# Optimization experiments

Hardware: AMD Instinct MI355X
Metric: run time of the kernel (lower is better)

The kernel has to match this reference:

```python
import jax, jax.numpy as jnp
import numpy as np

N = 50000
E = 800000
D_IN = 128
D_H = 128


def setup_inputs() -> dict:
    key = jax.random.key(0)
    ks = jax.random.split(key, 12)
    x = jax.random.normal(ks[0], (N, D_IN), dtype=jnp.float32)
    edge_index = jax.random.randint(ks[1], (2, E), 0, N, dtype=jnp.int32)
    reranker_scores = jax.random.uniform(ks[2], (N,), dtype=jnp.float32)
    s = 1.0 / np.sqrt(D_IN)
    # SAGEConv layer 1: lin_l (neighbors, with bias), lin_r (root, no bias)
    Wl1 = jax.random.uniform(ks[3], (D_H, D_IN), jnp.float32, -s, s)
    bl1 = jax.random.uniform(ks[4], (D_H,), jnp.float32, -s, s)
    Wr1 = jax.random.uniform(ks[5], (D_H, D_IN), jnp.float32, -s, s)
    # SAGEConv layer 2
    sh = 1.0 / np.sqrt(D_H)
    Wl2 = jax.random.uniform(ks[6], (D_H, D_H), jnp.float32, -sh, sh)
    bl2 = jax.random.uniform(ks[7], (D_H,), jnp.float32, -sh, sh)
    Wr2 = jax.random.uniform(ks[8], (D_H, D_H), jnp.float32, -sh, sh)
    # score head Linear(hidden, 1)
    Ws = jax.random.uniform(ks[9], (1, D_H), jnp.float32, -sh, sh)
    bs = jax.random.uniform(ks[10], (1,), jnp.float32, -sh, sh)
    alpha = jnp.asarray(0.65, dtype=jnp.float32)
    return {"x": x, "edge_index": edge_index, "reranker_scores": reranker_scores,
            "Wl1": Wl1, "bl1": bl1, "Wr1": Wr1,
            "Wl2": Wl2, "bl2": bl2, "Wr2": Wr2,
            "Ws": Ws, "bs": bs, "alpha": alpha}


def _sage_conv(h, src, dst, Wl, bl, Wr, n_nodes):
    # PyG SAGEConv, aggr='mean': out = lin_l(mean_j x_j) + lin_r(x_i)
    msgs = h[src]                                             # [E, d] gather
    agg = jax.ops.segment_sum(msgs, dst, num_segments=n_nodes)  # [N, d]
    cnt = jax.ops.segment_sum(jnp.ones((src.shape[0],), h.dtype), dst,
                              num_segments=n_nodes)           # [N]
    agg = agg / jnp.maximum(cnt, 1.0)[:, None]
    return agg @ Wl.T + bl + h @ Wr.T


def reference(x, edge_index, reranker_scores, Wl1, bl1, Wr1, Wl2, bl2, Wr2, Ws, bs, alpha):
    src, dst = edge_index[0], edge_index[1]
    h_in = x  # input_dim == hidden_dim -> identity residual
    h = x
    h = jax.nn.relu(_sage_conv(h, src, dst, Wl1, bl1, Wr1, N))  # dropout: eval (identity)
    h = jax.nn.relu(_sage_conv(h, src, dst, Wl2, bl2, Wr2, N))
    h = h + h_in
    gnn_scores = (h @ Ws.T + bs)[:, 0]                          # [N]
    a = jax.nn.sigmoid(alpha)
    return a * reranker_scores + (1.0 - a) * gnn_scores
```

## Files before the change

kernel.cpp:

```cpp
#include <hip/hip_runtime.h>

#define NN 50000
#define NE 800000
#define DD 128

#define NBUCK 196
#define EPB   2048
#define B1    391
#define CAP   5120
#define SLOT  40
#define CONVB 12500
#define PREPB 64

typedef __attribute__((ext_vector_type(8))) short short8v;
typedef __attribute__((ext_vector_type(4))) float float4v;

static __device__ __forceinline__ unsigned short f2b(float f) {
  union { float f; unsigned u; } v; v.f = f;
  unsigned r = v.u + 0x7fff + ((v.u >> 16) & 1);
  return (unsigned short)(r >> 16);
}
static __device__ __forceinline__ float b2f(unsigned short b) {
  union { unsigned u; float f; } v; v.u = ((unsigned)b) << 16;
  return v.f;
}

static __device__ __forceinline__ int excl_scan256(int v, int* ws) {
  int t = threadIdx.x, lane = t & 63, w = t >> 6;
  int s = v;
  #pragma unroll
  for (int off = 1; off < 64; off <<= 1) {
    int u = __shfl_up(s, off);
    if (lane >= off) s += u;
  }
  if (lane == 63) ws[w] = s;
  __syncthreads();
  int add = 0;
  #pragma unroll
  for (int k = 0; k < 3; ++k)
    if (k < w) add += ws[k];
  __syncthreads();
  return add + s - v;
}


__global__ __launch_bounds__(256) void k_prep(
    const int* __restrict__ src, const int* __restrict__ dst,
    int* __restrict__ ghist, unsigned* __restrict__ tmp,
    const float* __restrict__ x, const float* __restrict__ Wsc,
    unsigned char* __restrict__ xf8, float* __restrict__ xw,
    const float* __restrict__ Wl1, const float* __restrict__ Wr1,
    const float* __restrict__ Wl2, const float* __restrict__ Wr2,
    unsigned char* __restrict__ W1, unsigned char* __restrict__ W2) {
  __shared__ int hs[NBUCK];
  const int b = blockIdx.x;
  const int t = threadIdx.x;
  if (b < B1) {
    for (int i = t; i < NBUCK; i += 256) hs[i] = 0;
    __syncthreads();
    int base = b * EPB;
    for (int i = t; i < EPB; i += 256) {
      int e = base + i;
      if (e < NE) atomicAdd(&hs[dst[e] >> 8], 1);
    }
    __syncthreads();
    for (int i = t; i < NBUCK; i += 256) {
      ghist[b * NBUCK + i] = hs[i];
      hs[i] = 0;
    }
    __syncthreads();
    for (int i = t; i < EPB; i += 256) {
      int e = base + i;
      if (e < NE) {
        int d = dst[e];
        int j = d >> 8;
        int pos = atomicAdd(&hs[j], 1);
        if (pos < SLOT)
          tmp[((size_t)j * B1 + b) * SLOT + pos] =
              ((unsigned)(d & 255) << 20) | (unsigned)src[e];
      }
    }
  } else if (b < B1 + CONVB) {
    int node = (b - B1) * 4 + (t >> 6);
    int lane = t & 63;
    float2 v = *(const float2*)(x + (size_t)node * DD + lane * 2);
    int p8 = __builtin_amdgcn_cvt_pk_fp8_f32(v.x, v.y, 0, false);
    *(unsigned short*)(xf8 + (size_t)node * DD + lane * 2) = (unsigned short)p8;
    float p = v.x * Wsc[lane * 2] + v.y * Wsc[lane * 2 + 1];
    #pragma unroll
    for (int m = 1; m < 64; m <<= 1) p += __shfl_xor(p, m);
    if (lane == 0) xw[node] = p;
  } else {
    int idx0 = ((b - B1 - CONVB) * 256 + t) * 4;
    int half = idx0 >> 15;
    int i = idx0 & 32767;
    int o = i >> 8;
    int k = i & 255;
    const float* Wl = half ? Wl2 : Wl1;
    const float* Wr = half ? Wr2 : Wr1;
    const float* wsrc = (k < DD) ? (Wl + o * DD + k) : (Wr + o * DD + (k - DD));
    float4 v = *(const float4*)wsrc;
    unsigned wlo = (unsigned)(unsigned short)__builtin_amdgcn_cvt_pk_fp8_f32(v.x, v.y, 0, false);
    unsigned whi = (unsigned)(unsigned short)__builtin_amdgcn_cvt_pk_fp8_f32(v.z, v.w, 0, false);
    *(unsigned*)((half ? W2 : W1) + i) = wlo | (whi << 16);
  }
}


__global__ __launch_bounds__(256) void bucketsort(const unsigned* __restrict__ tmp,
                                                  const int* __restrict__ ghist,
                                                  int* __restrict__ rowbeg,
                                                  int* __restrict__ rowend,
                                                  int* __restrict__ col) {
  __shared__ unsigned vals[CAP];
  __shared__ int cnt[256];
  __shared__ int ws[4];
  __shared__ int tot;
  const int b = blockIdx.x, t = threadIdx.x;
  cnt[t] = 0;
  if (t == 0) tot = 0;
  __syncthreads();
  for (int blk = t; blk < B1; blk += 256) {
    int c = ghist[blk * NBUCK + b];
    if (c > SLOT) c = SLOT;
    if (c > 0) {
      int base = atomicAdd(&tot, c);
      const uint4* s = (const uint4*)(tmp + ((size_t)b * B1 + blk) * SLOT);
      for (int k4 = 0; k4 * 4 < c; ++k4) {
        uint4 v4 = s[k4];
        #pragma unroll
        for (int j = 0; j < 4; ++j) {
          int k = k4 * 4 + j;
          if (k < c && base + k < CAP) {
            unsigned v = (&v4.x)[j];
            vals[base + k] = v;
            atomicAdd(&cnt[v >> 20], 1);
          }
        }
      }
    }
  }
  __syncthreads();
  int n = tot;
  if (n > CAP) n = CAP;
  int c = cnt[t];
  int excl = excl_scan256(c, ws);
  int node = b * 256 + t;
  const int s0 = b * CAP;
  if (node < NN) {
    rowbeg[node] = s0 + excl;
    rowend[node] = s0 + excl + c;
  }
  cnt[t] = excl;
  __syncthreads();
  for (int i = t; i < n; i += 256) {
    unsigned v = vals[i];
    int pos = atomicAdd(&cnt[v >> 20], 1);
    col[s0 + pos] = (int)(v & 0xFFFFF);
  }
}


__global__ __launch_bounds__(256) void agg_fp8(const unsigned char* __restrict__ hf8,
                                               const int* __restrict__ rowbeg,
                                               const int* __restrict__ rowend,
                                               const int* __restrict__ col,
                                               unsigned char* __restrict__ aggf8) {
  int node = (blockIdx.x * 256 + threadIdx.x) >> 3;
  if (node >= NN) return;
  const int q = threadIdx.x & 7;
  const unsigned char* hb = hf8 + q * 16;
  int beg = rowbeg[node], end = rowend[node];
  float acc[16];
  #pragma unroll
  for (int k = 0; k < 16; ++k) acc[k] = 0.f;
  int e = beg;
  for (; e + 8 <= end; e += 8) {
    uint4 v[8];
    #pragma unroll
    for (int j = 0; j < 8; ++j)
      v[j] = *(const uint4*)(hb + (size_t)col[e + j] * DD);
    #pragma unroll
    for (int j = 0; j < 8; ++j) {
      #pragma unroll
      for (int d = 0; d < 4; ++d) {
        unsigned w = (&v[j].x)[d];
        auto lo = __builtin_amdgcn_cvt_pk_f32_fp8(w, false);
        auto hi = __builtin_amdgcn_cvt_pk_f32_fp8(w, true);
        acc[d * 4 + 0] += lo[0];
        acc[d * 4 + 1] += lo[1];
        acc[d * 4 + 2] += hi[0];
        acc[d * 4 + 3] += hi[1];
      }
    }
  }
  if (e < end) {
    uint4 v[8];
    #pragma unroll
    for (int j = 0; j < 8; ++j) {
      int idx = (e + j < end) ? (e + j) : (end - 1);
      v[j] = *(const uint4*)(hb + (size_t)col[idx] * DD);
    }
    #pragma unroll
    for (int j = 0; j < 8; ++j) {
      float m = (e + j < end) ? 1.f : 0.f;
      #pragma unroll
      for (int d = 0; d < 4; ++d) {
        unsigned w = (&v[j].x)[d];
        auto lo = __builtin_amdgcn_cvt_pk_f32_fp8(w, false);
        auto hi = __builtin_amdgcn_cvt_pk_f32_fp8(w, true);
        acc[d * 4 + 0] = fmaf(m, lo[0], acc[d * 4 + 0]);
        acc[d * 4 + 1] = fmaf(m, lo[1], acc[d * 4 + 1]);
        acc[d * 4 + 2] = fmaf(m, hi[0], acc[d * 4 + 2]);
        acc[d * 4 + 3] = fmaf(m, hi[1], acc[d * 4 + 3]);
      }
    }
  }
  float inv = 1.0f / fmaxf((float)(end - beg), 1.0f);
  uint4 o;
  unsigned* ow = &o.x;
  #pragma unroll
  for (int d = 0; d < 4; ++d) {
    unsigned wlo = (unsigned)(unsigned short)__builtin_amdgcn_cvt_pk_fp8_f32(
        acc[d * 4 + 0] * inv, acc[d * 4 + 1] * inv, 0, false);
    unsigned whi = (unsigned)(unsigned short)__builtin_amdgcn_cvt_pk_fp8_f32(
        acc[d * 4 + 2] * inv, acc[d * 4 + 3] * inv, 0, false);
    ow[d] = wlo | (whi << 16);
  }
  *(uint4*)(aggf8 + (size_t)node * DD + q * 16) = o;
}


template <bool SCORE>
__global__ __launch_bounds__(256) void linear_mfma(
    const unsigned char* __restrict__ aggf8, const unsigned char* __restrict__ hf8,
    const unsigned char* __restrict__ Wcat, const float* __restrict__ bl,
    unsigned char* __restrict__ hf8out,
    const float* __restrict__ Ws, const float* __restrict__ bsp,
    const float* __restrict__ alphap, const float* __restrict__ rr,
    const float* __restrict__ xw, float* __restrict__ out) {
  __shared__ unsigned char zl8[64 * 256];
  __shared__ float sbuf[64];

  const int t = threadIdx.x;
  const int wid = t >> 6;
  const int l = t & 63;
  const int lg = l >> 4;
  const int lm = l & 15;
  const int node0 = blockIdx.x * 64;
  const int nb = wid * 32;

  long bfr[2][8];
  #pragma unroll
  for (int nf = 0; nf < 2; ++nf)
    #pragma unroll
    for (int kt = 0; kt < 8; ++kt)
      bfr[nf][kt] = *(const long*)(Wcat + (size_t)(nb + nf * 16 + lm) * 256 + kt * 32 + lg * 8);

  if (SCORE && t < 64) sbuf[t] = 0.f;

  #pragma unroll
  for (int q = 0; q < 4; ++q) {
    int idx = q * 256 + t;
    int row = idx >> 4;
    int cp = idx & 15;
    int node = node0 + row; if (node >= NN) node = NN - 1;
    const unsigned char* srcp = (cp < 8)
        ? (aggf8 + (size_t)node * DD + cp * 16)
        : (hf8   + (size_t)node * DD + (cp - 8) * 16);
    uint4 w = *(const uint4*)srcp;
    int g0 = cp * 2, g1 = cp * 2 + 1;
    *(uint2*)(&zl8[row * 256 + (g0 ^ (row & 7)) * 8]) = make_uint2(w.x, w.y);
    *(uint2*)(&zl8[row * 256 + (g1 ^ (row & 7)) * 8]) = make_uint2(w.z, w.w);
  }
  __syncthreads();

  float4v acc[4][2];
  #pragma unroll
  for (int mf = 0; mf < 4; ++mf) {
    acc[mf][0] = (float4v){0.f, 0.f, 0.f, 0.f};
    acc[mf][1] = (float4v){0.f, 0.f, 0.f, 0.f};
  }

  #pragma unroll
  for (int kt = 0; kt < 8; ++kt) {
    long afr[4];
    #pragma unroll
    for (int mf = 0; mf < 4; ++mf) {
      int row = mf * 16 + lm;
      int g = (kt * 4 + lg) ^ (row & 7);
      afr[mf] = *(const long*)(&zl8[row * 256 + g * 8]);
    }
    #pragma unroll
    for (int mf = 0; mf < 4; ++mf) {
      acc[mf][0] = __builtin_amdgcn_mfma_f32_16x16x32_fp8_fp8(afr[mf], bfr[0][kt], acc[mf][0], 0, 0, 0);
      acc[mf][1] = __builtin_amdgcn_mfma_f32_16x16x32_fp8_fp8(afr[mf], bfr[1][kt], acc[mf][1], 0, 0, 0);
    }
  }

  const float b0 = bl[nb + lm];
  const float b1 = bl[nb + 16 + lm];

  if (!SCORE) {
    __syncthreads();
    unsigned short* zlo = (unsigned short*)zl8;
    #pragma unroll
    for (int mf = 0; mf < 4; ++mf) {
      #pragma unroll
      for (int r = 0; r < 4; ++r) {
        int row = mf * 16 + lg * 4 + r;
        zlo[row * 128 + nb + lm]      = f2b(fmaxf(acc[mf][0][r] + b0, 0.f));
        zlo[row * 128 + nb + 16 + lm] = f2b(fmaxf(acc[mf][1][r] + b1, 0.f));
      }
    }
    __syncthreads();
    #pragma unroll
    for (int i = 0; i < 2; ++i) {
      int idx = i * 256 + t;
      int row = idx >> 3;
      int c16 = idx & 7;
      int node = node0 + row;
      if (node < NN) {
        short8v v0 = *(const short8v*)(&zlo[row * 128 + c16 * 16]);
        short8v v1 = *(const short8v*)(&zlo[row * 128 + c16 * 16 + 8]);
        uint4 p8;
        unsigned* pw = &p8.x;
        #pragma unroll
        for (int k2 = 0; k2 < 2; ++k2) {
          const short8v& v = k2 ? v1 : v0;
          unsigned wlo = (unsigned)(unsigned short)__builtin_amdgcn_cvt_pk_fp8_f32(
              b2f((unsigned short)v[0]), b2f((unsigned short)v[1]), 0, false);
          unsigned whi = (unsigned)(unsigned short)__builtin_amdgcn_cvt_pk_fp8_f32(
              b2f((unsigned short)v[2]), b2f((unsigned short)v[3]), 0, false);
          pw[k2 * 2] = wlo | (whi << 16);
          wlo = (unsigned)(unsigned short)__builtin_amdgcn_cvt_pk_fp8_f32(
              b2f((unsigned short)v[4]), b2f((unsigned short)v[5]), 0, false);
          whi = (unsigned)(unsigned short)__builtin_amdgcn_cvt_pk_fp8_f32(
              b2f((unsigned short)v[6]), b2f((unsigned short)v[7]), 0, false);
          pw[k2 * 2 + 1] = wlo | (whi << 16);
        }
        *(uint4*)(hf8out + (size_t)node * DD + c16 * 16) = p8;
      }
    }
  } else {
    const float w0 = Ws[nb + lm];
    const float w1 = Ws[nb + 16 + lm];
    #pragma unroll
    for (int mf = 0; mf < 4; ++mf) {
      #pragma unroll
      for (int r = 0; r < 4; ++r) {
        float p = fmaxf(acc[mf][0][r] + b0, 0.f) * w0
                + fmaxf(acc[mf][1][r] + b1, 0.f) * w1;
        p += __shfl_xor(p, 1);
        p += __shfl_xor(p, 2);
        p += __shfl_xor(p, 4);
        p += __shfl_xor(p, 8);
        if (lm == 0) atomicAdd(&sbuf[mf * 16 + lg * 4 + r], p);
      }
    }
    __syncthreads();
    if (t < 64) {
      int node = node0 + t;
      if (node < NN) {
        float a = 1.f / (1.f + expf(-alphap[0]));
        float score = sbuf[t] + xw[node] + bsp[0];
        out[node] = a * rr[node] + (1.f - a) * score;
      }
    }
  }
}


extern "C" void kernel_launch(void* const* d_in, const int* in_sizes, int n_in,
                              void* d_out, int out_size, void* d_ws, size_t ws_size,
                              hipStream_t stream) {
  const float* x   = (const float*)d_in[0];
  const int*   ei  = (const int*)d_in[1];
  const float* rr  = (const float*)d_in[2];
  const float* Wl1 = (const float*)d_in[3];
  const float* bl1 = (const float*)d_in[4];
  const float* Wr1 = (const float*)d_in[5];
  const float* Wl2 = (const float*)d_in[6];
  const float* bl2 = (const float*)d_in[7];
  const float* Wr2 = (const float*)d_in[8];
  const float* Wsc = (const float*)d_in[9];
  const float* bs  = (const float*)d_in[10];
  const float* al  = (const float*)d_in[11];
  const int* srcv = ei;
  const int* dstv = ei + NE;
  float* out = (float*)d_out;

  size_t off = 0;
  auto nxt = [&](size_t bytes) {
    size_t cur = off; off += (bytes + 255) & ~(size_t)255; return cur;
  };
  int*            ghist  = (int*)((char*)d_ws + nxt((size_t)B1 * NBUCK * 4));
  int*            rowbeg = (int*)((char*)d_ws + nxt((size_t)NN * 4));
  int*            rowend = (int*)((char*)d_ws + nxt((size_t)NN * 4));
  int*            col    = (int*)((char*)d_ws + nxt((size_t)NBUCK * CAP * 4));
  unsigned*       tmp    = (unsigned*)((char*)d_ws + nxt((size_t)NBUCK * B1 * SLOT * 4));
  unsigned char*  aggf8  = (unsigned char*)((char*)d_ws + nxt((size_t)NN * DD));
  unsigned char*  xf8    = (unsigned char*)((char*)d_ws + nxt((size_t)NN * DD));
  unsigned char*  h1f8   = (unsigned char*)((char*)d_ws + nxt((size_t)NN * DD));
  unsigned char*  W1     = (unsigned char*)((char*)d_ws + nxt((size_t)DD * 256));
  unsigned char*  W2     = (unsigned char*)((char*)d_ws + nxt((size_t)DD * 256));
  float*          xw     = (float*)((char*)d_ws + nxt((size_t)NN * 4));

  k_prep<<<B1 + CONVB + PREPB, 256, 0, stream>>>(
      srcv, dstv, ghist, tmp, x, Wsc, xf8, xw, Wl1, Wr1, Wl2, Wr2, W1, W2);
  bucketsort<<<NBUCK, 256, 0, stream>>>(tmp, ghist, rowbeg, rowend, col);

  agg_fp8<<<(NN * 8 + 255) / 256, 256, 0, stream>>>(xf8, rowbeg, rowend, col, aggf8);
  linear_mfma<false><<<(NN + 63) / 64, 256, 0, stream>>>(
      aggf8, xf8, W1, bl1, h1f8, nullptr, nullptr, nullptr, nullptr, nullptr, nullptr);
  agg_fp8<<<(NN * 8 + 255) / 256, 256, 0, stream>>>(h1f8, rowbeg, rowend, col, aggf8);
  linear_mfma<true><<<(NN + 63) / 64, 256, 0, stream>>>(
      aggf8, h1f8, W2, bl2, nullptr, Wsc, bs, al, rr, xw, out);
}
```

Measured before the change: 91.51 us.

## Fuse neighbor mean aggregation into the MFMA linear kernel per layer

Merges the separate gather/mean aggregation kernel and the fp8 MFMA linear kernel into one kernel per layer. Each block now aggregates 32 nodes straight into shared memory, then runs the MFMA on them. This removes the aggf8 global round trip and two kernel launches. In exchange the tile shrinks to 32 rows, so each block reloads the weight fragments for half the work, and the gather latency now sits in front of the MFMA in the same block.

```diff
diff --git a/kernel.cpp b/kernel.cpp
--- a/kernel.cpp
+++ b/kernel.cpp
@@ -161,94 +161,106 @@
 }
 
 
-__global__ __launch_bounds__(256) void agg_fp8(const unsigned char* __restrict__ hf8,
-                                               const int* __restrict__ rowbeg,
-                                               const int* __restrict__ rowend,
-                                               const int* __restrict__ col,
-                                               unsigned char* __restrict__ aggf8) {
-  int node = (blockIdx.x * 256 + threadIdx.x) >> 3;
-  if (node >= NN) return;
-  const int q = threadIdx.x & 7;
-  const unsigned char* hb = hf8 + q * 16;
-  int beg = rowbeg[node], end = rowend[node];
-  float acc[16];
-  #pragma unroll
-  for (int k = 0; k < 16; ++k) acc[k] = 0.f;
-  int e = beg;
-  for (; e + 8 <= end; e += 8) {
-    uint4 v[8];
-    #pragma unroll
-    for (int j = 0; j < 8; ++j)
-      v[j] = *(const uint4*)(hb + (size_t)col[e + j] * DD);
-    #pragma unroll
-    for (int j = 0; j < 8; ++j) {
-      #pragma unroll
-      for (int d = 0; d < 4; ++d) {
-        unsigned w = (&v[j].x)[d];
-        auto lo = __builtin_amdgcn_cvt_pk_f32_fp8(w, false);
-        auto hi = __builtin_amdgcn_cvt_pk_f32_fp8(w, true);
-        acc[d * 4 + 0] += lo[0];
-        acc[d * 4 + 1] += lo[1];
-        acc[d * 4 + 2] += hi[0];
-        acc[d * 4 + 3] += hi[1];
-      }
-    }
-  }
-  if (e < end) {
-    uint4 v[8];
-    #pragma unroll
-    for (int j = 0; j < 8; ++j) {
-      int idx = (e + j < end) ? (e + j) : (end - 1);
-      v[j] = *(const uint4*)(hb + (size_t)col[idx] * DD);
-    }
-    #pragma unroll
-    for (int j = 0; j < 8; ++j) {
-      float m = (e + j < end) ? 1.f : 0.f;
-      #pragma unroll
-      for (int d = 0; d < 4; ++d) {
-        unsigned w = (&v[j].x)[d];
-        auto lo = __builtin_amdgcn_cvt_pk_f32_fp8(w, false);
-        auto hi = __builtin_amdgcn_cvt_pk_f32_fp8(w, true);
-        acc[d * 4 + 0] = fmaf(m, lo[0], acc[d * 4 + 0]);
-        acc[d * 4 + 1] = fmaf(m, lo[1], acc[d * 4 + 1]);
-        acc[d * 4 + 2] = fmaf(m, hi[0], acc[d * 4 + 2]);
-        acc[d * 4 + 3] = fmaf(m, hi[1], acc[d * 4 + 3]);
-      }
-    }
-  }
-  float inv = 1.0f / fmaxf((float)(end - beg), 1.0f);
-  uint4 o;
-  unsigned* ow = &o.x;
-  #pragma unroll
-  for (int d = 0; d < 4; ++d) {
-    unsigned wlo = (unsigned)(unsigned short)__builtin_amdgcn_cvt_pk_fp8_f32(
-        acc[d * 4 + 0] * inv, acc[d * 4 + 1] * inv, 0, false);
-    unsigned whi = (unsigned)(unsigned short)__builtin_amdgcn_cvt_pk_fp8_f32(
-        acc[d * 4 + 2] * inv, acc[d * 4 + 3] * inv, 0, false);
-    ow[d] = wlo | (whi << 16);
-  }
-  *(uint4*)(aggf8 + (size_t)node * DD + q * 16) = o;
-}
-
-
 template <bool SCORE>
-__global__ __launch_bounds__(256) void linear_mfma(
-    const unsigned char* __restrict__ aggf8, const unsigned char* __restrict__ hf8,
+__global__ __launch_bounds__(256) void fused_layer(
+    const unsigned char* __restrict__ hf8,
+    const int* __restrict__ rowbeg, const int* __restrict__ rowend,
+    const int* __restrict__ col,
     const unsigned char* __restrict__ Wcat, const float* __restrict__ bl,
     unsigned char* __restrict__ hf8out,
     const float* __restrict__ Ws, const float* __restrict__ bsp,
     const float* __restrict__ alphap, const float* __restrict__ rr,
     const float* __restrict__ xw, float* __restrict__ out) {
-  __shared__ unsigned char zl8[64 * 256];
-  __shared__ float sbuf[64];
+  __shared__ unsigned char zl8[32 * 256];
+  __shared__ float sbuf[32];
 
   const int t = threadIdx.x;
   const int wid = t >> 6;
   const int l = t & 63;
   const int lg = l >> 4;
   const int lm = l & 15;
-  const int node0 = blockIdx.x * 64;
+  const int node0 = blockIdx.x * 32;
   const int nb = wid * 32;
+
+  if (SCORE && t < 32) sbuf[t] = 0.f;
+
+  {
+    const int row = t >> 3;
+    const int q = t & 7;
+    int node = node0 + row;
+    int nc = node < NN ? node : NN - 1;
+    const unsigned char* hb = hf8 + q * 16;
+    int beg = rowbeg[nc], end = rowend[nc];
+    float acc[16];
+    #pragma unroll
+    for (int k = 0; k < 16; ++k) acc[k] = 0.f;
+    int e = beg;
+    for (; e + 8 <= end; e += 8) {
+      uint4 v[8];
+      #pragma unroll
+      for (int j = 0; j < 8; ++j)
+        v[j] = *(const uint4*)(hb + (size_t)col[e + j] * DD);
+      #pragma unroll
+      for (int j = 0; j < 8; ++j) {
+        #pragma unroll
+        for (int d = 0; d < 4; ++d) {
+          unsigned w = (&v[j].x)[d];
+          auto lo = __builtin_amdgcn_cvt_pk_f32_fp8(w, false);
+          auto hi = __builtin_amdgcn_cvt_pk_f32_fp8(w, true);
+          acc[d * 4 + 0] += lo[0];
+          acc[d * 4 + 1] += lo[1];
+          acc[d * 4 + 2] += hi[0];
+          acc[d * 4 + 3] += hi[1];
+        }
+      }
+    }
+    if (e < end) {
+      uint4 v[8];
+      #pragma unroll
+      for (int j = 0; j < 8; ++j) {
+        int idx = (e + j < end) ? (e + j) : (end - 1);
+        v[j] = *(const uint4*)(hb + (size_t)col[idx] * DD);
+      }
+      #pragma unroll
+      for (int j = 0; j < 8; ++j) {
+        float m = (e + j < end) ? 1.f : 0.f;
+        #pragma unroll
+        for (int d = 0; d < 4; ++d) {
+          unsigned w = (&v[j].x)[d];
+          auto lo = __builtin_amdgcn_cvt_pk_f32_fp8(w, false);
+          auto hi = __builtin_amdgcn_cvt_pk_f32_fp8(w, true);
+          acc[d * 4 + 0] = fmaf(m, lo[0], acc[d * 4 + 0]);
+          acc[d * 4 + 1] = fmaf(m, lo[1], acc[d * 4 + 1]);
+          acc[d * 4 + 2] = fmaf(m, hi[0], acc[d * 4 + 2]);
+          acc[d * 4 + 3] = fmaf(m, hi[1], acc[d * 4 + 3]);
+        }
+      }
+    }
+    float inv = 1.0f / fmaxf((float)(end - beg), 1.0f);
+    unsigned ow[4];
+    #pragma unroll
+    for (int d = 0; d < 4; ++d) {
+      unsigned wlo = (unsigned)(unsigned short)__builtin_amdgcn_cvt_pk_fp8_f32(
+          acc[d * 4 + 0] * inv, acc[d * 4 + 1] * inv, 0, false);
+      unsigned whi = (unsigned)(unsigned short)__builtin_amdgcn_cvt_pk_fp8_f32(
+          acc[d * 4 + 2] * inv, acc[d * 4 + 3] * inv, 0, false);
+      ow[d] = wlo | (whi << 16);
+    }
+    int g0 = 2 * q, g1 = 2 * q + 1;
+    *(uint2*)(&zl8[row * 256 + (g0 ^ (row & 7)) * 8]) = make_uint2(ow[0], ow[1]);
+    *(uint2*)(&zl8[row * 256 + (g1 ^ (row & 7)) * 8]) = make_uint2(ow[2], ow[3]);
+  }
+
+  {
+    const int row = t >> 3;
+    const int cp = 8 + (t & 7);
+    int node = node0 + row; if (node >= NN) node = NN - 1;
+    uint4 w = *(const uint4*)(hf8 + (size_t)node * DD + (cp - 8) * 16);
+    int g0 = cp * 2, g1 = cp * 2 + 1;
+    *(uint2*)(&zl8[row * 256 + (g0 ^ (row & 7)) * 8]) = make_uint2(w.x, w.y);
+    *(uint2*)(&zl8[row * 256 + (g1 ^ (row & 7)) * 8]) = make_uint2(w.z, w.w);
+  }
+  __syncthreads();
 
   long bfr[2][8];
   #pragma unroll
@@ -257,42 +269,24 @@
     for (int kt = 0; kt < 8; ++kt)
       bfr[nf][kt] = *(const long*)(Wcat + (size_t)(nb + nf * 16 + lm) * 256 + kt * 32 + lg * 8);
 
-  if (SCORE && t < 64) sbuf[t] = 0.f;
-
+  float4v acc[2][2];
   #pragma unroll
-  for (int q = 0; q < 4; ++q) {
-    int idx = q * 256 + t;
-    int row = idx >> 4;
-    int cp = idx & 15;
-    int node = node0 + row; if (node >= NN) node = NN - 1;
-    const unsigned char* srcp = (cp < 8)
-        ? (aggf8 + (size_t)node * DD + cp * 16)
-        : (hf8   + (size_t)node * DD + (cp - 8) * 16);
-    uint4 w = *(const uint4*)srcp;
-    int g0 = cp * 2, g1 = cp * 2 + 1;
-    *(uint2*)(&zl8[row * 256 + (g0 ^ (row & 7)) * 8]) = make_uint2(w.x, w.y);
-    *(uint2*)(&zl8[row * 256 + (g1 ^ (row & 7)) * 8]) = make_uint2(w.z, w.w);
-  }
-  __syncthreads();
-
-  float4v acc[4][2];
-  #pragma unroll
-  for (int mf = 0; mf < 4; ++mf) {
+  for (int mf = 0; mf < 2; ++mf) {
     acc[mf][0] = (float4v){0.f, 0.f, 0.f, 0.f};
     acc[mf][1] = (float4v){0.f, 0.f, 0.f, 0.f};
   }
 
   #pragma unroll
   for (int kt = 0; kt < 8; ++kt) {
-    long afr[4];
-    #pragma unroll
-    for (int mf = 0; mf < 4; ++mf) {
+    long afr[2];
+    #pragma unroll
+    for (int mf = 0; mf < 2; ++mf) {
       int row = mf * 16 + lm;
       int g = (kt * 4 + lg) ^ (row & 7);
       afr[mf] = *(const long*)(&zl8[row * 256 + g * 8]);
     }
     #pragma unroll
-    for (int mf = 0; mf < 4; ++mf) {
+    for (int mf = 0; mf < 2; ++mf) {
       acc[mf][0] = __builtin_amdgcn_mfma_f32_16x16x32_fp8_fp8(afr[mf], bfr[0][kt], acc[mf][0], 0, 0, 0);
       acc[mf][1] = __builtin_amdgcn_mfma_f32_16x16x32_fp8_fp8(afr[mf], bfr[1][kt], acc[mf][1], 0, 0, 0);
     }
@@ -305,7 +299,7 @@
     __syncthreads();
     unsigned short* zlo = (unsigned short*)zl8;
     #pragma unroll
-    for (int mf = 0; mf < 4; ++mf) {
+    for (int mf = 0; mf < 2; ++mf) {
       #pragma unroll
       for (int r = 0; r < 4; ++r) {
         int row = mf * 16 + lg * 4 + r;
@@ -314,11 +308,9 @@
       }
     }
     __syncthreads();
-    #pragma unroll
-    for (int i = 0; i < 2; ++i) {
-      int idx = i * 256 + t;
-      int row = idx >> 3;
-      int c16 = idx & 7;
+    {
+      int row = t >> 3;
+      int c16 = t & 7;
       int node = node0 + row;
       if (node < NN) {
         short8v v0 = *(const short8v*)(&zlo[row * 128 + c16 * 16]);
@@ -346,7 +338,7 @@
     const float w0 = Ws[nb + lm];
     const float w1 = Ws[nb + 16 + lm];
     #pragma unroll
-    for (int mf = 0; mf < 4; ++mf) {
+    for (int mf = 0; mf < 2; ++mf) {
       #pragma unroll
       for (int r = 0; r < 4; ++r) {
         float p = fmaxf(acc[mf][0][r] + b0, 0.f) * w0
@@ -359,7 +351,7 @@
       }
     }
     __syncthreads();
-    if (t < 64) {
+    if (t < 32) {
       int node = node0 + t;
       if (node < NN) {
         float a = 1.f / (1.f + expf(-alphap[0]));
@@ -399,7 +391,6 @@
   int*            rowend = (int*)((char*)d_ws + nxt((size_t)NN * 4));
   int*            col    = (int*)((char*)d_ws + nxt((size_t)NBUCK * CAP * 4));
   unsigned*       tmp    = (unsigned*)((char*)d_ws + nxt((size_t)NBUCK * B1 * SLOT * 4));
-  unsigned char*  aggf8  = (unsigned char*)((char*)d_ws + nxt((size_t)NN * DD));
   unsigned char*  xf8    = (unsigned char*)((char*)d_ws + nxt((size_t)NN * DD));
   unsigned char*  h1f8   = (unsigned char*)((char*)d_ws + nxt((size_t)NN * DD));
   unsigned char*  W1     = (unsigned char*)((char*)d_ws + nxt((size_t)DD * 256));
@@ -410,10 +401,10 @@
       srcv, dstv, ghist, tmp, x, Wsc, xf8, xw, Wl1, Wr1, Wl2, Wr2, W1, W2);
   bucketsort<<<NBUCK, 256, 0, stream>>>(tmp, ghist, rowbeg, rowend, col);
 
-  agg_fp8<<<(NN * 8 + 255) / 256, 256, 0, stream>>>(xf8, rowbeg, rowend, col, aggf8);
-  linear_mfma<false><<<(NN + 63) / 64, 256, 0, stream>>>(
-      aggf8, xf8, W1, bl1, h1f8, nullptr, nullptr, nullptr, nullptr, nullptr, nullptr);
-  agg_fp8<<<(NN * 8 + 255) / 256, 256, 0, stream>>>(h1f8, rowbeg, rowend, col, aggf8);
-  linear_mfma<true><<<(NN + 63) / 64, 256, 0, stream>>>(
-      aggf8, h1f8, W2, bl2, nullptr, Wsc, bs, al, rr, xw, out);
-}
+  fused_layer<false><<<(NN + 31) / 32, 256, 0, stream>>>(
+      xf8, rowbeg, rowend, col, W1, bl1, h1f8,
+      nullptr, nullptr, nullptr, nullptr, nullptr, nullptr);
+  fused_layer<true><<<(NN + 31) / 32, 256, 0, stream>>>(
+      h1f8, rowbeg, rowend, col, W2, bl2, nullptr,
+      Wsc, bs, al, rr, xw, out);
+}
```

Result: slower. 103.5 us (+13.1%).
